# Performance work log

Measured on AMD Instinct MI355X. Metric: run time of the kernel, lower is better.

Reference implementation:

```python
import jax, jax.numpy as jnp
import numpy as np


def dct_matrix(n):
    # orthonormal DCT-II matrix, matches scipy.fftpack.dct(norm='ortho')
    k = jnp.arange(n, dtype=jnp.float32)[:, None]
    i = jnp.arange(n, dtype=jnp.float32)[None, :]
    D = jnp.cos(jnp.pi * (2.0 * i + 1.0) * k / (2.0 * n))
    s = jnp.where(k == 0, jnp.sqrt(1.0 / n), jnp.sqrt(2.0 / n))
    return (D * s).astype(jnp.float32)


def mad_mask(h, w):
    eps = 1e-10
    v1 = int(min(h, w) * 0.1)
    v2 = int(min(h, w) * 0.7)
    v3 = min(h, w)
    xy = jnp.maximum(jnp.arange(h, dtype=jnp.float32)[:, None],
                     jnp.arange(w, dtype=jnp.float32)[None, :])
    m = jnp.where(xy <= v1, 1.0 - xy / (v1 + eps) * 0.95,
        jnp.where(xy <= v2, 0.01,
        jnp.where(xy <= v3, (xy - v2) / (v3 - v2) * 0.3, 0.5)))
    return m.astype(jnp.float32)


def setup_inputs() -> dict:
    key = jax.random.key(0)
    ks = jax.random.split(key, 8)
    num_layers, token_length, C = 24, 100, 1024
    N, B = 1024, 32  # h = w = 32
    patch = 16
    val = np.sqrt(6.0 / float(3 * patch * patch + C))
    feats = jax.random.normal(ks[0], (1 + N, B, C), dtype=jnp.float32)
    learnable_tokens = jax.random.uniform(ks[1], (num_layers, token_length, C),
                                          minval=-val, maxval=val, dtype=jnp.float32)
    lim = 1.0 / np.sqrt(C)
    W_t2f = jax.random.uniform(ks[2], (C, C), minval=-lim, maxval=lim, dtype=jnp.float32)
    b_t2f = jax.random.uniform(ks[3], (C,), minval=-lim, maxval=lim, dtype=jnp.float32)
    W_df = jax.random.uniform(ks[4], (C, C), minval=-lim, maxval=lim, dtype=jnp.float32)
    b_df = jax.random.uniform(ks[5], (C,), minval=-lim, maxval=lim, dtype=jnp.float32)
    return {
        'feats': feats,
        'layer': 5,
        'learnable_tokens': learnable_tokens,
        'scale': jnp.float32(0.001),
        'W_t2f': W_t2f,
        'b_t2f': b_t2f,
        'W_df': W_df,
        'b_df': b_df,
    }


def reference(feats, layer, learnable_tokens, scale, W_t2f, b_t2f, W_df, b_df):
    # has_cls_token=True, batch_first=False (defaults)
    cls_tok, x = feats[:1], feats[1:]          # [1,B,C], [N,B,C]
    N, B, C = x.shape
    h = int(np.sqrt(N)); w = h
    # NOTE: original does a raw reshape (N,B,C) -> (B,C,h,w); replicate faithfully.
    ximg = x.reshape(B, C, h, w)
    # --- MAD_decompose: 2D orthonormal DCT-II per (b, c) image ---
    D = dct_matrix(h)
    feat_dct = jnp.einsum('ik,bckl,jl->bcij', D, ximg, D)
    mask = mad_mask(h, w)                      # [h,w]
    cal = feat_dct * (1.0 - mask)              # high-frequency (causal) part
    cal = cal.reshape(N, B, C)                 # raw reshape as in torch code
    # --- forward_delta_feat ---
    tokens = learnable_tokens[layer]           # [M,C]
    attn = jnp.einsum('nbc,mc->nbm', cal, tokens) * (C ** -0.5)
    attn = jax.nn.softmax(attn, axis=-1)
    t2f = tokens[1:] @ W_t2f.T + b_t2f         # [M-1,C]
    df = jnp.einsum('nbm,mc->nbc', attn[:, :, 1:], t2f)
    df = (df + cal) @ W_df.T + b_df            # [N,B,C]
    # --- MAD_compose_fast: ifft2 approximation of IDCT, clamp to [0,255] ---
    fc = df.reshape(B, C, h, w).astype(jnp.complex64)
    out = jnp.clip(jnp.real(jnp.fft.ifft2(fc, norm='ortho')), 0.0, 255.0)
    out = out.reshape(N, B, C).astype(jnp.float32)
    x = x + out * scale
    return jnp.concatenate([cls_tok, x], axis=0)
```

## Files before the change

kernel.cpp:

```cpp
#include <hip/hip_runtime.h>

typedef unsigned short u16;
typedef u16 ushort8 __attribute__((ext_vector_type(8)));
typedef u16 ushort4v __attribute__((ext_vector_type(4)));
typedef __bf16 bf16x8 __attribute__((ext_vector_type(8)));
typedef float f32x4 __attribute__((ext_vector_type(4)));

#define PI_F 3.14159265358979323846f

__device__ __forceinline__ u16 f2bf(float f) {
  union { float f; unsigned int u; } v; v.f = f;
  unsigned int r = v.u + 0x7fffu + ((v.u >> 16) & 1u);
  return (u16)(r >> 16);
}
__device__ __forceinline__ float bf2f(u16 u) {
  union { unsigned int u; float f; } v; v.u = ((unsigned int)u) << 16;
  return v.f;
}

__device__ __forceinline__ void gload16(const u16* g, u16* l) {
  __builtin_amdgcn_global_load_lds((const __attribute__((address_space(1))) void*)g,
                                   (__attribute__((address_space(3))) void*)l, 16, 0, 0);
}

__device__ __forceinline__ void stage_tile(const u16* __restrict__ G, int ld, int row0, int k0,
                                           u16* lds, int wid, int lane) {
  int seg = wid * 32;
  const u16* gp = G + (size_t)(row0 + seg + (lane >> 2)) * ld + k0 + (lane & 3) * 8;
  gload16(gp, lds + seg * 32);
  gload16(gp + (size_t)16 * ld, lds + (seg + 16) * 32);
}

#define WAIT_VM(N) asm volatile("s_waitcnt vmcnt(" #N ")" ::: "memory")
#define RAW_BARRIER() asm volatile("s_barrier" ::: "memory")

__device__ __forceinline__ float im_val(int r, int c) {
  float xy = (float)(r > c ? r : c);
  float m = (xy <= 3.0f) ? (1.0f - xy * (0.95f / 3.0f))
           : ((xy <= 22.0f) ? 0.01f : ((xy - 22.0f) * 0.03f));
  return 1.0f - m;
}
__device__ __forceinline__ float dct_val(int r, int c) {
  int a = ((2 * c + 1) * r) & 127;
  float s = (r == 0) ? 0.17677669529663687f : 0.25f;
  return cosf((float)a * (PI_F / 64.0f)) * s;
}

__device__ void mdct_row(const float* __restrict__ row, u16* __restrict__ dst, float* sm, int t) {
  float* Ms = sm; float* T1 = sm + 1056; float* Dsh = sm + 2112;
  for (int i = t; i < 1024; i += 256) {
    int r = i >> 5, c = i & 31;
    Dsh[r * 33 + c] = dct_val(r, c);
    Ms[r * 33 + c] = row[i] * im_val(r, c);
  }
  __syncthreads();
  int k = t >> 3, l0 = (t & 7) * 4;
  float a0 = 0, a1 = 0, a2 = 0, a3 = 0;
  #pragma unroll 8
  for (int i = 0; i < 32; ++i) {
    float d = Dsh[i * 33 + k];
    const float* mr = &Ms[i * 33 + l0];
    a0 += d * mr[0]; a1 += d * mr[1]; a2 += d * mr[2]; a3 += d * mr[3];
  }
  T1[k * 33 + l0 + 0] = a0; T1[k * 33 + l0 + 1] = a1;
  T1[k * 33 + l0 + 2] = a2; T1[k * 33 + l0 + 3] = a3;
  __syncthreads();
  float b0 = 0, b1 = 0, b2 = 0, b3 = 0;
  #pragma unroll 8
  for (int j = 0; j < 32; ++j) {
    float u = T1[k * 33 + j];
    b0 += u * Dsh[j * 33 + l0 + 0];
    b1 += u * Dsh[j * 33 + l0 + 1];
    b2 += u * Dsh[j * 33 + l0 + 2];
    b3 += u * Dsh[j * 33 + l0 + 3];
  }
  ushort4v o;
  o[0] = f2bf(b0); o[1] = f2bf(b1); o[2] = f2bf(b2); o[3] = f2bf(b3);
  *(ushort4v*)(dst + k * 32 + l0) = o;
}

__global__ __launch_bounds__(256) void k_stage1(const float* __restrict__ feats,
                                                const float* __restrict__ lt, const int* __restrict__ layerp,
                                                const float* __restrict__ Wt2f,
                                                const float* __restrict__ Wdf, const float* __restrict__ bdf,
                                                u16* __restrict__ xb, u16* __restrict__ wt_bf,
                                                u16* __restrict__ tok_bf, u16* __restrict__ A2,
                                                float* __restrict__ outp,
                                                float* __restrict__ weff_f, u16* __restrict__ weff_bf,
                                                float* __restrict__ beff, u16* __restrict__ tok2) {
  __shared__ __align__(16) float sm[8448];
  int bid = blockIdx.x, t = threadIdx.x;
  if (bid < 2048) {
    int tid = bid * 256 + t;
    int L = *layerp;
    const float4* in4 = (const float4*)(feats + 32768);
    ushort4v* xb4 = (ushort4v*)xb;
    #pragma unroll
    for (int rep = 0; rep < 16; ++rep) {
      int j = tid + rep * 524288;
      float4 v = in4[j];
      ushort4v o;
      o[0] = f2bf(v.x); o[1] = f2bf(v.y); o[2] = f2bf(v.z); o[3] = f2bf(v.w);
      xb4[j] = o;
    }
    ((ushort8*)A2)[tid] = (ushort8){0,0,0,0,0,0,0,0};
    if (tid < 262144) {
      float4 v = ((const float4*)Wt2f)[tid];
      ushort4v o;
      o[0] = f2bf(v.x); o[1] = f2bf(v.y); o[2] = f2bf(v.z); o[3] = f2bf(v.w);
      ((ushort4v*)wt_bf)[tid] = o;
    }
    if (tid < 32768) {
      outp[tid] = feats[tid];
      int m = tid >> 8;
      ushort4v o = (ushort4v){0,0,0,0};
      if (m < 99) {
        float4 v = *(const float4*)(lt + (size_t)L * 102400 + (size_t)(m + 1) * 1024 + (tid & 255) * 4);
        o[0] = f2bf(v.x); o[1] = f2bf(v.y); o[2] = f2bf(v.z); o[3] = f2bf(v.w);
      }
      ((ushort4v*)tok_bf)[tid] = o;
    }
    return;
  }
  int b2 = bid - 2048;
  if (b2 < 512) {
    float* In = sm;
    float* Uc = sm + 2112;
    float* Us = sm + 4224;
    float* Csh = sm + 6336;
    float* Ssh = sm + 7392;
    int c0 = b2 * 2;
    for (int i = t; i < 1024; i += 256) {
      int r = i >> 5, c = i & 31;
      float ang = (float)((r * c) & 31) * (PI_F / 16.0f);
      Csh[r * 33 + c] = cosf(ang); Ssh[r * 33 + c] = sinf(ang);
    }
    { int cc = t & 1, v0 = t >> 1;
      for (int v = v0; v < 1024; v += 128)
        In[cc * 1056 + (v >> 5) * 33 + (v & 31)] = Wdf[(size_t)v * 1024 + c0 + cc]; }
    __syncthreads();
    int cc = t >> 7, L7 = t & 127, p = L7 & 31, h = L7 >> 5;
    for (int j = h * 8; j < h * 8 + 8; ++j) {
      float ac = 0, as = 0;
      #pragma unroll 8
      for (int i = 0; i < 32; ++i) {
        float m = In[cc * 1056 + i * 33 + j];
        ac += Csh[p * 33 + i] * m;
        as += Ssh[p * 33 + i] * m;
      }
      Uc[cc * 1056 + p * 33 + j] = ac;
      Us[cc * 1056 + p * 33 + j] = as;
    }
    __syncthreads();
    for (int q = h * 8; q < h * 8 + 8; ++q) {
      float acc = 0;
      #pragma unroll 8
      for (int j = 0; j < 32; ++j)
        acc += Uc[cc * 1056 + p * 33 + j] * Csh[q * 33 + j] -
               Us[cc * 1056 + p * 33 + j] * Ssh[q * 33 + j];
      float val = acc * 0.03125f;
      size_t idx = (size_t)(p * 32 + q) * 1024 + c0 + cc;
      weff_f[idx] = val;
      weff_bf[idx] = f2bf(val);
    }
  } else if (b2 == 512) {
    float* Bsh = sm; float* Uc = sm + 1056; float* Us = sm + 2112;
    float* Csh = sm + 3168; float* Ssh = sm + 4224;
    for (int i = t; i < 1024; i += 256) {
      int r = i >> 5, c = i & 31;
      float ang = (float)((r * c) & 31) * (PI_F / 16.0f);
      Csh[r * 33 + c] = cosf(ang); Ssh[r * 33 + c] = sinf(ang);
      Bsh[r * 33 + c] = bdf[i];
    }
    __syncthreads();
    for (int idx = t; idx < 1024; idx += 256) {
      int p = idx >> 5, j = idx & 31;
      float ac = 0, as = 0;
      #pragma unroll 8
      for (int i = 0; i < 32; ++i) {
        float m = Bsh[i * 33 + j];
        ac += Csh[p * 33 + i] * m;
        as += Ssh[p * 33 + i] * m;
      }
      Uc[p * 33 + j] = ac; Us[p * 33 + j] = as;
    }
    __syncthreads();
    for (int idx = t; idx < 1024; idx += 256) {
      int p = idx >> 5, q = idx & 31;
      float acc = 0;
      #pragma unroll 8
      for (int jj = 0; jj < 32; ++jj)
        acc += Uc[p * 33 + jj] * Csh[q * 33 + jj] - Us[p * 33 + jj] * Ssh[q * 33 + jj];
      beff[idx] = acc * 0.03125f;
    }
  } else {
    int p = b2 - 513;
    if (p >= 100) {
      *(ushort4v*)(tok2 + (size_t)p * 1024 + t * 4) = (ushort4v){0,0,0,0};
      return;
    }
    mdct_row(lt + (size_t)(*layerp) * 102400 + (size_t)p * 1024, tok2 + (size_t)p * 1024, sm, t);
  }
}

template <int NT>
__device__ __forceinline__ void gemm128_core(const u16* __restrict__ A, int lda,
                                             const u16* __restrict__ B, int ldb,
                                             int g0, int c0, u16* smem,
                                             f32x4 (&acc)[4][4], int wid, int lane) {
  int wr = wid >> 1, wc = wid & 1, cl = lane & 15, rg = lane >> 4;
  stage_tile(A, lda, g0, 0, smem, wid, lane);
  stage_tile(B, ldb, c0, 0, smem + 12288, wid, lane);
  stage_tile(A, lda, g0, 32, smem + 4096, wid, lane);
  stage_tile(B, ldb, c0, 32, smem + 16384, wid, lane);
  int cur = 0;
  #pragma unroll 1
  for (int kt = 0; kt < NT; ++kt) {
    if (kt == NT - 1) { WAIT_VM(0); } else { WAIT_VM(4); }
    RAW_BARRIER();
    if (kt + 2 < NT) {
      int slot = (cur == 0) ? 2 : cur - 1;
      stage_tile(A, lda, g0, (kt + 2) * 32, smem + slot * 4096, wid, lane);
      stage_tile(B, ldb, c0, (kt + 2) * 32, smem + 12288 + slot * 4096, wid, lane);
    }
    const u16* pa = smem + cur * 4096;
    const u16* pb = smem + 12288 + cur * 4096;
    bf16x8 af[4], bv[4];
    #pragma unroll
    for (int mf = 0; mf < 4; mf++)
      af[mf] = *(const bf16x8*)(pa + (wr * 64 + mf * 16 + cl) * 32 + rg * 8);
    #pragma unroll
    for (int nf = 0; nf < 4; nf++)
      bv[nf] = *(const bf16x8*)(pb + (wc * 64 + nf * 16 + cl) * 32 + rg * 8);
    #pragma unroll
    for (int mf = 0; mf < 4; mf++)
      #pragma unroll
      for (int nf = 0; nf < 4; nf++)
        acc[mf][nf] = __builtin_amdgcn_mfma_f32_16x16x32_bf16(af[mf], bv[nf], acc[mf][nf], 0, 0, 0);
    cur = (cur == 2) ? 0 : cur + 1;
  }
}

__global__ __launch_bounds__(256) void k_stage2(const float* __restrict__ weff_f,
                                                const u16* __restrict__ tok_bf, const u16* __restrict__ wt_bf,
                                                const float* __restrict__ bt2f,
                                                const u16* __restrict__ xb, const u16* __restrict__ tok2,
                                                u16* __restrict__ w2, u16* __restrict__ t2f,
                                                u16* __restrict__ A2) {
  __shared__ __align__(16) u16 smem[24576];
  int bid = blockIdx.x, t = threadIdx.x;
  int lane = t & 63, wid = t >> 6;
  if (bid < 1024) {
    mdct_row(weff_f + (size_t)bid * 1024, w2 + (size_t)bid * 1024, (float*)smem, t);
  } else if (bid < 1032) {
    int bn = bid - 1024;
    int wr = wid >> 1, wc = wid & 1, cl = lane & 15, rg = lane >> 4;
    f32x4 acc[4][4];
    #pragma unroll
    for (int i = 0; i < 4; i++)
      #pragma unroll
      for (int j = 0; j < 4; j++) acc[i][j] = (f32x4){0.f,0.f,0.f,0.f};
    gemm128_core<32>(tok_bf, 1024, wt_bf, 1024, 0, bn * 128, smem, acc, wid, lane);
    #pragma unroll
    for (int mf = 0; mf < 4; mf++)
      #pragma unroll
      for (int nf = 0; nf < 4; nf++) {
        int col = bn * 128 + wc * 64 + nf * 16 + cl;
        #pragma unroll
        for (int r = 0; r < 4; r++) {
          int row = wr * 64 + mf * 16 + rg * 4 + r;
          t2f[(size_t)row * 1024 + col] = (row < 99) ? f2bf(acc[mf][nf][r] + bt2f[col]) : (u16)0;
        }
      }
  } else {
    int g0 = (bid - 1032) * 128;
    int cl = lane & 15, rg = lane >> 4;
    f32x4 acc[2][7];
    #pragma unroll
    for (int i = 0; i < 2; i++)
      #pragma unroll
      for (int j = 0; j < 7; j++) acc[i][j] = (f32x4){0.f,0.f,0.f,0.f};
    stage_tile(xb, 1024, g0, 0, smem, wid, lane);
    stage_tile(tok2, 1024, 0, 0, smem + 12288, wid, lane);
    stage_tile(xb, 1024, g0, 32, smem + 4096, wid, lane);
    stage_tile(tok2, 1024, 0, 32, smem + 16384, wid, lane);
    int cur = 0;
    #pragma unroll 1
    for (int kt = 0; kt < 32; ++kt) {
      if (kt == 31) { WAIT_VM(0); } else { WAIT_VM(4); }
      RAW_BARRIER();
      if (kt + 2 < 32) {
        int slot = (cur == 0) ? 2 : cur - 1;
        stage_tile(xb, 1024, g0, (kt + 2) * 32, smem + slot * 4096, wid, lane);
        stage_tile(tok2, 1024, 0, (kt + 2) * 32, smem + 12288 + slot * 4096, wid, lane);
      }
      const u16* pa = smem + cur * 4096;
      const u16* pb = smem + 12288 + cur * 4096;
      bf16x8 a0 = *(const bf16x8*)(pa + (wid * 32 + cl) * 32 + rg * 8);
      bf16x8 a1 = *(const bf16x8*)(pa + (wid * 32 + 16 + cl) * 32 + rg * 8);
      #pragma unroll
      for (int nf = 0; nf < 7; nf++) {
        bf16x8 bv = *(const bf16x8*)(pb + (nf * 16 + cl) * 32 + rg * 8);
        acc[0][nf] = __builtin_amdgcn_mfma_f32_16x16x32_bf16(a0, bv, acc[0][nf], 0, 0, 0);
        acc[1][nf] = __builtin_amdgcn_mfma_f32_16x16x32_bf16(a1, bv, acc[1][nf], 0, 0, 0);
      }
      cur = (cur == 2) ? 0 : cur + 1;
    }
    #pragma unroll
    for (int mf = 0; mf < 2; mf++) {
      #pragma unroll
      for (int r = 0; r < 4; r++) {
        int grow = g0 + wid * 32 + mf * 16 + rg * 4 + r;
        float v[7];
        float mx = -1e30f;
        #pragma unroll
        for (int nf = 0; nf < 7; nf++) {
          int m = nf * 16 + cl;
          v[nf] = acc[mf][nf][r] * 0.03125f;
          if (m < 100) mx = fmaxf(mx, v[nf]);
        }
        #pragma unroll
        for (int d = 1; d < 16; d <<= 1) mx = fmaxf(mx, __shfl_xor(mx, d));
        float s = 0;
        #pragma unroll
        for (int nf = 0; nf < 7; nf++) {
          int m = nf * 16 + cl;
          float e = (m < 100) ? __expf(v[nf] - mx) : 0.0f;
          v[nf] = e; s += e;
        }
        #pragma unroll
        for (int d = 1; d < 16; d <<= 1) s += __shfl_xor(s, d);
        float inv = 1.0f / s;
        #pragma unroll
        for (int nf = 0; nf < 7; nf++) {
          int m = nf * 16 + cl;
          if (m >= 1 && m < 100) A2[(size_t)grow * 128 + (m - 1)] = f2bf(v[nf] * inv);
        }
      }
    }
  }
}

__global__ __launch_bounds__(256) void k_gt(const u16* __restrict__ weff_bf, const u16* __restrict__ t2f,
                                            u16* __restrict__ Gt) {
  __shared__ __align__(16) u16 smem[24576];
  int bid = blockIdx.x, t = threadIdx.x;
  int lane = t & 63, wid = t >> 6;
  int wr = wid >> 1, wc = wid & 1, cl = lane & 15, rg = lane >> 4;
  f32x4 acc[4][4];
  #pragma unroll
  for (int i = 0; i < 4; i++)
    #pragma unroll
    for (int j = 0; j < 4; j++) acc[i][j] = (f32x4){0.f,0.f,0.f,0.f};
  gemm128_core<32>(weff_bf, 1024, t2f, 1024, bid * 128, 0, smem, acc, wid, lane);
  #pragma unroll
  for (int mf = 0; mf < 4; mf++)
    #pragma unroll
    for (int nf = 0; nf < 4; nf++) {
      int col = wc * 64 + nf * 16 + cl;
      #pragma unroll
      for (int r = 0; r < 4; r++) {
        int row = bid * 128 + wr * 64 + mf * 16 + rg * 4 + r;
        Gt[(size_t)row * 128 + col] = f2bf(acc[mf][nf][r]);
      }
    }
}

__global__ __launch_bounds__(512, 4) void k_main(const u16* __restrict__ xb, const u16* __restrict__ w2,
                                                 const u16* __restrict__ a2, const u16* __restrict__ gt,
                                                 const float* __restrict__ beff, const float* __restrict__ feats,
                                                 const float* __restrict__ scalep, float* __restrict__ outf) {
  __shared__ __align__(16) u16 smem[36864];
  int tid = threadIdx.x, lane = tid & 63, wid = tid >> 6;
  int wr = wid >> 2, wc = wid & 3;
  int cl = lane & 15, rg = lane >> 4;
  int bid = blockIdx.x;
  int swz = (bid & 7) * 128 + (bid >> 3);
  int bm = swz >> 3, bn = swz & 7;
  int g0 = bm * 256, c0 = bn * 128;

  f32x4 acc[8][2];
  #pragma unroll
  for (int i = 0; i < 8; i++)
    #pragma unroll
    for (int j = 0; j < 2; j++) acc[i][j] = (f32x4){0.f,0.f,0.f,0.f};

  const int NT = 36;

  int offA[8], offB[2];
  #pragma unroll
  for (int mf = 0; mf < 8; ++mf) {
    int r = wr * 128 + mf * 16 + cl;
    int lrow = r >> 1;
    offA[mf] = lrow * 64 + (((((r & 1) << 2) | rg) ^ (lrow & 7)) << 3);
  }
  #pragma unroll
  for (int nf = 0; nf < 2; ++nf) {
    int r = wc * 32 + nf * 16 + cl;
    int lrow = r >> 1;
    offB[nf] = lrow * 64 + (((((r & 1) << 2) | rg) ^ (lrow & 7)) << 3);
  }

  auto issueA = [&](int t) {
    u16* R = smem + (t % 3) * 8192;
    const u16* G = (t < 32) ? xb : a2;
    int ld = (t < 32) ? 1024 : 128;
    int k0 = (t < 32) ? t * 32 : (t - 32) * 32;
    #pragma unroll
    for (int p = 0; p < 2; ++p) {
      int lrow = p * 64 + wid * 8 + (lane >> 3);
      int c2 = (lane & 7) ^ (lrow & 7);
      const u16* src = G + (size_t)(g0 + 2 * lrow + (c2 >> 2)) * ld + k0 + (c2 & 3) * 8;
      gload16(src, R + (p * 64 + wid * 8) * 64);
    }
  };
  auto issueB = [&](int t) {
    u16* R = smem + 24576 + (t % 3) * 4096;
    const u16* G = (t < 32) ? w2 : gt;
    int ld = (t < 32) ? 1024 : 128;
    int k0 = (t < 32) ? t * 32 : (t - 32) * 32;
    int lrow = wid * 8 + (lane >> 3);
    int c2 = (lane & 7) ^ (lrow & 7);
    const u16* src = G + (size_t)(c0 + 2 * lrow + (c2 >> 2)) * ld + k0 + (c2 & 3) * 8;
    gload16(src, R + (wid * 8) * 64);
  };

  issueA(0); issueB(0);
  issueA(1); issueB(1);

  #pragma unroll 1
  for (int t = 0; t < NT; ++t) {
    if (t == NT - 1) { WAIT_VM(0); } else { WAIT_VM(3); }
    RAW_BARRIER();
    int slot = t % 3;
    const u16* pa = smem + slot * 8192;
    const u16* pb = smem + 24576 + slot * 4096;
    bf16x8 bv[2];
    #pragma unroll
    for (int nf = 0; nf < 2; ++nf) bv[nf] = *(const bf16x8*)(pb + offB[nf]);
    if (t + 2 < NT) { issueA(t + 2); issueB(t + 2); }
    #pragma unroll
    for (int mg = 0; mg < 2; ++mg) {
      bf16x8 af[4];
      #pragma unroll
      for (int m4 = 0; m4 < 4; ++m4) af[m4] = *(const bf16x8*)(pa + offA[mg * 4 + m4]);
      __builtin_amdgcn_s_setprio(1);
      #pragma unroll
      for (int m4 = 0; m4 < 4; ++m4)
        #pragma unroll
        for (int nf = 0; nf < 2; ++nf)
          acc[mg * 4 + m4][nf] = __builtin_amdgcn_mfma_f32_16x16x32_bf16(af[m4], bv[nf], acc[mg * 4 + m4][nf], 0, 0, 0);
      __builtin_amdgcn_s_setprio(0);
    }
  }

  float sc = *scalep;
  #pragma unroll
  for (int mf = 0; mf < 8; mf++) {
    #pragma unroll
    for (int nf = 0; nf < 2; nf++) {
      int col = c0 + wc * 32 + nf * 16 + cl;
      #pragma unroll
      for (int r = 0; r < 4; r++) {
        int row = g0 + wr * 128 + mf * 16 + rg * 4 + r;
        size_t idx = (size_t)row * 1024 + col;
        float val = acc[mf][nf][r] + beff[col];
        float rr = fminf(fmaxf(val, 0.f), 255.f);
        outf[32768 + idx] = feats[32768 + idx] + rr * sc;
      }
    }
  }
}

extern "C" void kernel_launch(void* const* d_in, const int* in_sizes, int n_in,
                              void* d_out, int out_size, void* d_ws, size_t ws_size,
                              hipStream_t stream) {
  const float* feats  = (const float*)d_in[0];
  const int*   layerp = (const int*)d_in[1];
  const float* lt     = (const float*)d_in[2];
  const float* scalep = (const float*)d_in[3];
  const float* Wt2f   = (const float*)d_in[4];
  const float* bt2f   = (const float*)d_in[5];
  const float* Wdf    = (const float*)d_in[6];
  const float* bdf    = (const float*)d_in[7];
  float* outp = (float*)d_out;

  char* ws = (char*)d_ws;
  float* beff   = (float*)(ws + 0);
  float* weff_f = (float*)(ws + 65536);
  u16* weff_bf = (u16*)(ws + 4259840);
  u16* w2      = (u16*)(ws + 6356992);
  u16* tok_bf  = (u16*)(ws + 8454144);
  u16* wt_bf   = (u16*)(ws + 8716288);
  u16* tok2    = (u16*)(ws + 10813440);
  u16* t2f     = (u16*)(ws + 11075584);
  u16* Gt      = (u16*)(ws + 11337728);
  u16* A2      = (u16*)(ws + 11599872);
  u16* xb      = (u16*)(ws + 19988480);

  k_stage1<<<2689, 256, 0, stream>>>(feats, lt, layerp, Wt2f, Wdf, bdf,
                                     xb, wt_bf, tok_bf, A2, outp, weff_f, weff_bf, beff, tok2);
  k_stage2<<<1288, 256, 0, stream>>>(weff_f, tok_bf, wt_bf, bt2f, xb, tok2, w2, t2f, A2);
  k_gt<<<8, 256, 0, stream>>>(weff_bf, t2f, Gt);
  k_main<<<1024, 512, 0, stream>>>(xb, w2, A2, Gt, beff, feats, scalep, outp);
}
```

Before: 224.6 us.

## Reshuffle pre-kernels to overlap t2f GEMM with feature conversion and drop k_gt

The weight-only preprocessing (Weff DCT, bias, token DCT, Wt2f/token bf16 conversion) moves into a first kernel. The tokens@Wt2f GEMM now runs alongside the large feats-to-bf16 conversion. The Gt GEMM folds into stage2 next to the w2 DCT rows, which removes the nearly idle 8-block k_gt launch. The main GEMM loop also replaces its lambda-based address computation with precomputed, incrementing global pointers to cut per-iteration integer work.

New measurement: 226.3 us, median of 4. About the same (+0.8%).

```diff
diff --git a/kernel.cpp b/kernel.cpp
--- a/kernel.cpp
+++ b/kernel.cpp
@@ -79,57 +79,18 @@
   *(ushort4v*)(dst + k * 32 + l0) = o;
 }
 
-__global__ __launch_bounds__(256) void k_stage1(const float* __restrict__ feats,
-                                                const float* __restrict__ lt, const int* __restrict__ layerp,
-                                                const float* __restrict__ Wt2f,
-                                                const float* __restrict__ Wdf, const float* __restrict__ bdf,
-                                                u16* __restrict__ xb, u16* __restrict__ wt_bf,
-                                                u16* __restrict__ tok_bf, u16* __restrict__ A2,
-                                                float* __restrict__ outp,
-                                                float* __restrict__ weff_f, u16* __restrict__ weff_bf,
-                                                float* __restrict__ beff, u16* __restrict__ tok2) {
+__global__ __launch_bounds__(256) void k_pre(const float* __restrict__ lt, const int* __restrict__ layerp,
+                                             const float* __restrict__ Wt2f,
+                                             const float* __restrict__ Wdf, const float* __restrict__ bdf,
+                                             float* __restrict__ weff_f, u16* __restrict__ weff_bf,
+                                             float* __restrict__ beff, u16* __restrict__ tok2,
+                                             u16* __restrict__ wt_bf, u16* __restrict__ tok_bf) {
   __shared__ __align__(16) float sm[8448];
   int bid = blockIdx.x, t = threadIdx.x;
-  if (bid < 2048) {
-    int tid = bid * 256 + t;
-    int L = *layerp;
-    const float4* in4 = (const float4*)(feats + 32768);
-    ushort4v* xb4 = (ushort4v*)xb;
-    #pragma unroll
-    for (int rep = 0; rep < 16; ++rep) {
-      int j = tid + rep * 524288;
-      float4 v = in4[j];
-      ushort4v o;
-      o[0] = f2bf(v.x); o[1] = f2bf(v.y); o[2] = f2bf(v.z); o[3] = f2bf(v.w);
-      xb4[j] = o;
-    }
-    ((ushort8*)A2)[tid] = (ushort8){0,0,0,0,0,0,0,0};
-    if (tid < 262144) {
-      float4 v = ((const float4*)Wt2f)[tid];
-      ushort4v o;
-      o[0] = f2bf(v.x); o[1] = f2bf(v.y); o[2] = f2bf(v.z); o[3] = f2bf(v.w);
-      ((ushort4v*)wt_bf)[tid] = o;
-    }
-    if (tid < 32768) {
-      outp[tid] = feats[tid];
-      int m = tid >> 8;
-      ushort4v o = (ushort4v){0,0,0,0};
-      if (m < 99) {
-        float4 v = *(const float4*)(lt + (size_t)L * 102400 + (size_t)(m + 1) * 1024 + (tid & 255) * 4);
-        o[0] = f2bf(v.x); o[1] = f2bf(v.y); o[2] = f2bf(v.z); o[3] = f2bf(v.w);
-      }
-      ((ushort4v*)tok_bf)[tid] = o;
-    }
-    return;
-  }
-  int b2 = bid - 2048;
-  if (b2 < 512) {
-    float* In = sm;
-    float* Uc = sm + 2112;
-    float* Us = sm + 4224;
-    float* Csh = sm + 6336;
-    float* Ssh = sm + 7392;
-    int c0 = b2 * 2;
+  if (bid < 512) {
+    float* In = sm; float* Uc = sm + 2112; float* Us = sm + 4224;
+    float* Csh = sm + 6336; float* Ssh = sm + 7392;
+    int c0 = bid * 2;
     for (int i = t; i < 1024; i += 256) {
       int r = i >> 5, c = i & 31;
       float ang = (float)((r * c) & 31) * (PI_F / 16.0f);
@@ -163,7 +124,7 @@
       weff_f[idx] = val;
       weff_bf[idx] = f2bf(val);
     }
-  } else if (b2 == 512) {
+  } else if (bid == 512) {
     float* Bsh = sm; float* Uc = sm + 1056; float* Us = sm + 2112;
     float* Csh = sm + 3168; float* Ssh = sm + 4224;
     for (int i = t; i < 1024; i += 256) {
@@ -193,13 +154,29 @@
         acc += Uc[p * 33 + jj] * Csh[q * 33 + jj] - Us[p * 33 + jj] * Ssh[q * 33 + jj];
       beff[idx] = acc * 0.03125f;
     }
-  } else {
-    int p = b2 - 513;
+  } else if (bid < 641) {
+    int p = bid - 513;
     if (p >= 100) {
       *(ushort4v*)(tok2 + (size_t)p * 1024 + t * 4) = (ushort4v){0,0,0,0};
       return;
     }
     mdct_row(lt + (size_t)(*layerp) * 102400 + (size_t)p * 1024, tok2 + (size_t)p * 1024, sm, t);
+  } else if (bid < 1665) {
+    int idx = (bid - 641) * 256 + t;
+    float4 v = ((const float4*)Wt2f)[idx];
+    ushort4v o;
+    o[0] = f2bf(v.x); o[1] = f2bf(v.y); o[2] = f2bf(v.z); o[3] = f2bf(v.w);
+    ((ushort4v*)wt_bf)[idx] = o;
+  } else {
+    int idx = (bid - 1665) * 256 + t;
+    int L = *layerp;
+    int m = idx >> 8;
+    ushort4v o = (ushort4v){0,0,0,0};
+    if (m < 99) {
+      float4 v = *(const float4*)(lt + (size_t)L * 102400 + (size_t)(m + 1) * 1024 + (idx & 255) * 4);
+      o[0] = f2bf(v.x); o[1] = f2bf(v.y); o[2] = f2bf(v.z); o[3] = f2bf(v.w);
+    }
+    ((ushort4v*)tok_bf)[idx] = o;
   }
 }
 
@@ -241,11 +218,55 @@
   }
 }
 
+__global__ __launch_bounds__(256) void k_prep(const float* __restrict__ feats,
+                                              const u16* __restrict__ tok_bf, const u16* __restrict__ wt_bf,
+                                              const float* __restrict__ bt2f,
+                                              u16* __restrict__ xb, u16* __restrict__ A2,
+                                              float* __restrict__ outp, u16* __restrict__ t2f) {
+  __shared__ __align__(16) u16 smem[24576];
+  int bid = blockIdx.x, t = threadIdx.x;
+  if (bid < 2048) {
+    int tid = bid * 256 + t;
+    const float4* in4 = (const float4*)(feats + 32768);
+    ushort4v* xb4 = (ushort4v*)xb;
+    #pragma unroll
+    for (int rep = 0; rep < 16; ++rep) {
+      int j = tid + rep * 524288;
+      float4 v = in4[j];
+      ushort4v o;
+      o[0] = f2bf(v.x); o[1] = f2bf(v.y); o[2] = f2bf(v.z); o[3] = f2bf(v.w);
+      xb4[j] = o;
+    }
+    ((ushort8*)A2)[tid] = (ushort8){0,0,0,0,0,0,0,0};
+    if (tid < 32768) outp[tid] = feats[tid];
+    return;
+  }
+  int bn = bid - 2048;
+  int lane = t & 63, wid = t >> 6;
+  int wr = wid >> 1, wc = wid & 1, cl = lane & 15, rg = lane >> 4;
+  f32x4 acc[4][4];
+  #pragma unroll
+  for (int i = 0; i < 4; i++)
+    #pragma unroll
+    for (int j = 0; j < 4; j++) acc[i][j] = (f32x4){0.f,0.f,0.f,0.f};
+  gemm128_core<32>(tok_bf, 1024, wt_bf, 1024, 0, bn * 128, smem, acc, wid, lane);
+  #pragma unroll
+  for (int mf = 0; mf < 4; mf++)
+    #pragma unroll
+    for (int nf = 0; nf < 4; nf++) {
+      int col = bn * 128 + wc * 64 + nf * 16 + cl;
+      #pragma unroll
+      for (int r = 0; r < 4; r++) {
+        int row = wr * 64 + mf * 16 + rg * 4 + r;
+        t2f[(size_t)row * 1024 + col] = (row < 99) ? f2bf(acc[mf][nf][r] + bt2f[col]) : (u16)0;
+      }
+    }
+}
+
 __global__ __launch_bounds__(256) void k_stage2(const float* __restrict__ weff_f,
-                                                const u16* __restrict__ tok_bf, const u16* __restrict__ wt_bf,
-                                                const float* __restrict__ bt2f,
+                                                const u16* __restrict__ weff_bf, const u16* __restrict__ t2f,
                                                 const u16* __restrict__ xb, const u16* __restrict__ tok2,
-                                                u16* __restrict__ w2, u16* __restrict__ t2f,
+                                                u16* __restrict__ w2, u16* __restrict__ Gt,
                                                 u16* __restrict__ A2) {
   __shared__ __align__(16) u16 smem[24576];
   int bid = blockIdx.x, t = threadIdx.x;
@@ -253,23 +274,23 @@
   if (bid < 1024) {
     mdct_row(weff_f + (size_t)bid * 1024, w2 + (size_t)bid * 1024, (float*)smem, t);
   } else if (bid < 1032) {
-    int bn = bid - 1024;
+    int gb = bid - 1024;
     int wr = wid >> 1, wc = wid & 1, cl = lane & 15, rg = lane >> 4;
     f32x4 acc[4][4];
     #pragma unroll
     for (int i = 0; i < 4; i++)
       #pragma unroll
       for (int j = 0; j < 4; j++) acc[i][j] = (f32x4){0.f,0.f,0.f,0.f};
-    gemm128_core<32>(tok_bf, 1024, wt_bf, 1024, 0, bn * 128, smem, acc, wid, lane);
+    gemm128_core<32>(weff_bf, 1024, t2f, 1024, gb * 128, 0, smem, acc, wid, lane);
     #pragma unroll
     for (int mf = 0; mf < 4; mf++)
       #pragma unroll
       for (int nf = 0; nf < 4; nf++) {
-        int col = bn * 128 + wc * 64 + nf * 16 + cl;
+        int col = wc * 64 + nf * 16 + cl;
         #pragma unroll
         for (int r = 0; r < 4; r++) {
-          int row = wr * 64 + mf * 16 + rg * 4 + r;
-          t2f[(size_t)row * 1024 + col] = (row < 99) ? f2bf(acc[mf][nf][r] + bt2f[col]) : (u16)0;
+          int row = gb * 128 + wr * 64 + mf * 16 + rg * 4 + r;
+          Gt[(size_t)row * 128 + col] = f2bf(acc[mf][nf][r]);
         }
       }
   } else {
@@ -341,31 +362,6 @@
   }
 }
 
-__global__ __launch_bounds__(256) void k_gt(const u16* __restrict__ weff_bf, const u16* __restrict__ t2f,
-                                            u16* __restrict__ Gt) {
-  __shared__ __align__(16) u16 smem[24576];
-  int bid = blockIdx.x, t = threadIdx.x;
-  int lane = t & 63, wid = t >> 6;
-  int wr = wid >> 1, wc = wid & 1, cl = lane & 15, rg = lane >> 4;
-  f32x4 acc[4][4];
-  #pragma unroll
-  for (int i = 0; i < 4; i++)
-    #pragma unroll
-    for (int j = 0; j < 4; j++) acc[i][j] = (f32x4){0.f,0.f,0.f,0.f};
-  gemm128_core<32>(weff_bf, 1024, t2f, 1024, bid * 128, 0, smem, acc, wid, lane);
-  #pragma unroll
-  for (int mf = 0; mf < 4; mf++)
-    #pragma unroll
-    for (int nf = 0; nf < 4; nf++) {
-      int col = wc * 64 + nf * 16 + cl;
-      #pragma unroll
-      for (int r = 0; r < 4; r++) {
-        int row = bid * 128 + wr * 64 + mf * 16 + rg * 4 + r;
-        Gt[(size_t)row * 128 + col] = f2bf(acc[mf][nf][r]);
-      }
-    }
-}
-
 __global__ __launch_bounds__(512, 4) void k_main(const u16* __restrict__ xb, const u16* __restrict__ w2,
                                                  const u16* __restrict__ a2, const u16* __restrict__ gt,
                                                  const float* __restrict__ beff, const float* __restrict__ feats,
@@ -401,44 +397,44 @@
     offB[nf] = lrow * 64 + (((((r & 1) << 2) | rg) ^ (lrow & 7)) << 3);
   }
 
-  auto issueA = [&](int t) {
-    u16* R = smem + (t % 3) * 8192;
-    const u16* G = (t < 32) ? xb : a2;
-    int ld = (t < 32) ? 1024 : 128;
-    int k0 = (t < 32) ? t * 32 : (t - 32) * 32;
-    #pragma unroll
-    for (int p = 0; p < 2; ++p) {
-      int lrow = p * 64 + wid * 8 + (lane >> 3);
-      int c2 = (lane & 7) ^ (lrow & 7);
-      const u16* src = G + (size_t)(g0 + 2 * lrow + (c2 >> 2)) * ld + k0 + (c2 & 3) * 8;
-      gload16(src, R + (p * 64 + wid * 8) * 64);
-    }
-  };
-  auto issueB = [&](int t) {
-    u16* R = smem + 24576 + (t % 3) * 4096;
-    const u16* G = (t < 32) ? w2 : gt;
-    int ld = (t < 32) ? 1024 : 128;
-    int k0 = (t < 32) ? t * 32 : (t - 32) * 32;
-    int lrow = wid * 8 + (lane >> 3);
-    int c2 = (lane & 7) ^ (lrow & 7);
-    const u16* src = G + (size_t)(c0 + 2 * lrow + (c2 >> 2)) * ld + k0 + (c2 & 3) * 8;
-    gload16(src, R + (wid * 8) * 64);
-  };
-
-  issueA(0); issueB(0);
-  issueA(1); issueB(1);
-
+  int lrA0 = wid * 8 + (lane >> 3);
+  int lrA1 = 64 + lrA0;
+  int c2A0 = (lane & 7) ^ (lrA0 & 7);
+  int c2A1 = (lane & 7) ^ (lrA1 & 7);
+  const u16* pa0 = xb + (size_t)(g0 + 2 * lrA0 + (c2A0 >> 2)) * 1024 + (c2A0 & 3) * 8;
+  const u16* pa1 = xb + (size_t)(g0 + 2 * lrA1 + (c2A1 >> 2)) * 1024 + (c2A1 & 3) * 8;
+  const u16* pb  = w2 + (size_t)(c0 + 2 * lrA0 + (c2A0 >> 2)) * 1024 + (c2A0 & 3) * 8;
+  u16* dA0 = smem + (wid * 8) * 64;
+  u16* dA1 = smem + (64 + wid * 8) * 64;
+  u16* dB  = smem + 24576 + (wid * 8) * 64;
+
+  gload16(pa0, dA0); gload16(pa1, dA1); gload16(pb, dB);
+  pa0 += 32; pa1 += 32; pb += 32;
+  gload16(pa0, dA0 + 8192); gload16(pa1, dA1 + 8192); gload16(pb, dB + 4096);
+  pa0 += 32; pa1 += 32; pb += 32;
+
+  int sc_cur = 0, sc_iss = 2;
   #pragma unroll 1
   for (int t = 0; t < NT; ++t) {
     if (t == NT - 1) { WAIT_VM(0); } else { WAIT_VM(3); }
     RAW_BARRIER();
-    int slot = t % 3;
-    const u16* pa = smem + slot * 8192;
-    const u16* pb = smem + 24576 + slot * 4096;
+    const u16* pa = smem + sc_cur * 8192;
+    const u16* pbs = smem + 24576 + sc_cur * 4096;
     bf16x8 bv[2];
-    #pragma unroll
-    for (int nf = 0; nf < 2; ++nf) bv[nf] = *(const bf16x8*)(pb + offB[nf]);
-    if (t + 2 < NT) { issueA(t + 2); issueB(t + 2); }
+    bv[0] = *(const bf16x8*)(pbs + offB[0]);
+    bv[1] = *(const bf16x8*)(pbs + offB[1]);
+    if (t < NT - 2) {
+      if (t == 30) {
+        pa0 = a2 + (size_t)(g0 + 2 * lrA0 + (c2A0 >> 2)) * 128 + (c2A0 & 3) * 8;
+        pa1 = a2 + (size_t)(g0 + 2 * lrA1 + (c2A1 >> 2)) * 128 + (c2A1 & 3) * 8;
+        pb  = gt + (size_t)(c0 + 2 * lrA0 + (c2A0 >> 2)) * 128 + (c2A0 & 3) * 8;
+      }
+      gload16(pa0, dA0 + sc_iss * 8192);
+      gload16(pa1, dA1 + sc_iss * 8192);
+      gload16(pb,  dB  + sc_iss * 4096);
+      pa0 += 32; pa1 += 32; pb += 32;
+      sc_iss = (sc_iss == 2) ? 0 : sc_iss + 1;
+    }
     #pragma unroll
     for (int mg = 0; mg < 2; ++mg) {
       bf16x8 af[4];
@@ -452,6 +448,7 @@
           acc[mg * 4 + m4][nf] = __builtin_amdgcn_mfma_f32_16x16x32_bf16(af[m4], bv[nf], acc[mg * 4 + m4][nf], 0, 0, 0);
       __builtin_amdgcn_s_setprio(0);
     }
+    sc_cur = (sc_cur == 2) ? 0 : sc_cur + 1;
   }
 
   float sc = *scalep;
@@ -498,9 +495,9 @@
   u16* A2      = (u16*)(ws + 11599872);
   u16* xb      = (u16*)(ws + 19988480);
 
-  k_stage1<<<2689, 256, 0, stream>>>(feats, lt, layerp, Wt2f, Wdf, bdf,
-                                     xb, wt_bf, tok_bf, A2, outp, weff_f, weff_bf, beff, tok2);
-  k_stage2<<<1288, 256, 0, stream>>>(weff_f, tok_bf, wt_bf, bt2f, xb, tok2, w2, t2f, A2);
-  k_gt<<<8, 256, 0, stream>>>(weff_bf, t2f, Gt);
+  k_pre<<<1793, 256, 0, stream>>>(lt, layerp, Wt2f, Wdf, bdf,
+                                  weff_f, weff_bf, beff, tok2, wt_bf, tok_bf);
+  k_prep<<<2056, 256, 0, stream>>>(feats, tok_bf, wt_bf, bt2f, xb, A2, outp, t2f);
+  k_stage2<<<1288, 256, 0, stream>>>(weff_f, weff_bf, t2f, xb, tok2, w2, Gt, A2);
   k_main<<<1024, 512, 0, stream>>>(xb, w2, A2, Gt, beff, feats, scalep, outp);
 }
```
